# Kernel tuning notes

Measured on AMD Instinct MI355X. Metric: run time of the kernel, lower is better.

The kernel has to match this reference:

```python
import jax, jax.numpy as jnp
import numpy as np

N = 8192      # batched tree nodes
HD = 1024     # head_dim
D = 1024      # input_dim == output_dim


def _xavier(key, shape):
    fan_out, fan_in = shape
    std = (2.0 / (fan_in + fan_out)) ** 0.5
    return std * jax.random.normal(key, shape, dtype=jnp.float32)


def setup_inputs() -> dict:
    key = jax.random.key(0)
    ks = jax.random.split(key, 16)
    inp = {
        "x_l": jax.random.normal(ks[0], (N, HD), jnp.float32),
        "h_l": jax.random.normal(ks[1], (N, D), jnp.float32),
        "c_l": jax.random.normal(ks[2], (N, D), jnp.float32),
        "x_r": jax.random.normal(ks[3], (N, HD), jnp.float32),
        "h_r": jax.random.normal(ks[4], (N, D), jnp.float32),
        "c_r": jax.random.normal(ks[5], (N, D), jnp.float32),
        # Linear weights stored torch-style [out, in]; biases init to 0 per reset_parameters
        "W_i": _xavier(ks[6], (D, 4 * D)),   "b_i": jnp.zeros((D,), jnp.float32),
        "W_fl": _xavier(ks[7], (D, 4 * D)),  "b_fl": jnp.zeros((D,), jnp.float32),
        "W_fr": _xavier(ks[8], (D, 4 * D)),  "b_fr": jnp.zeros((D,), jnp.float32),
        "W_xin": _xavier(ks[9], (4 * D, HD)),
        "W_o": _xavier(ks[10], (D, 3 * D)),  "b_o": jnp.zeros((D,), jnp.float32),
        "W_z": _xavier(ks[11], (HD, 2 * HD)), "b_z": jnp.zeros((HD,), jnp.float32),
        "W_g": _xavier(ks[12], (D, 2 * D)),  "b_g": jnp.zeros((D,), jnp.float32),
        "dim": 1,
    }
    return inp


def reference(x_l, h_l, c_l, x_r, h_r, c_r,
              W_i, b_i, W_fl, b_fl, W_fr, b_fr, W_xin,
              W_o, b_o, W_z, b_z, W_g, b_g, dim):
    lin = lambda x, W, b: x @ W.T + b
    # gating to merge child head representations
    child_x = jnp.concatenate([x_l, x_r], axis=dim)
    z_t = jax.nn.sigmoid(lin(child_x, W_z, b_z))
    x_t = z_t * x_l + (1.0 - z_t) * x_r
    # input projection (no bias), split into 4 gates
    x_in_t = x_t @ W_xin.T                      # [N, 4D]
    x_i, x_f, x_o, x_g = jnp.split(x_in_t, 4, axis=dim)
    concat_input = jnp.concatenate([h_l, h_r, c_l, c_r], axis=dim)  # [N, 4D]
    i_t = jax.nn.sigmoid(lin(concat_input, W_i, b_i) + x_i)
    f_lt = jax.nn.sigmoid(lin(concat_input, W_fl, b_fl) + x_f)
    f_rt = jax.nn.sigmoid(lin(concat_input, W_fr, b_fr) + x_f)
    concat_g = jnp.concatenate([h_l, h_r], axis=dim)
    g_t = jnp.tanh(x_g + lin(concat_g, W_g, b_g))  # dropout p=0 -> identity
    c_t = f_lt * c_l + f_rt * c_r + i_t * g_t
    concat_o = jnp.concatenate([h_l, h_r, c_t], axis=dim)
    o_t = jax.nn.sigmoid(x_o + lin(concat_o, W_o, b_o))
    h_t = o_t * jnp.tanh(c_t)
    return (x_t, h_t, c_t)
```

## Files before the change

kernel.cpp:

```cpp
#include <hip/hip_runtime.h>
#include <math.h>

#define NROWS 8192

typedef __attribute__((ext_vector_type(8))) short short8;
typedef __attribute__((ext_vector_type(4))) float f32x4;
typedef __attribute__((ext_vector_type(4))) int i32x4;

__device__ __forceinline__ unsigned short f2bf(float f) {
  union { float f; unsigned int u; } v; v.f = f;
  unsigned int u = v.u;
  unsigned int r = (u + 0x7fffu + ((u >> 16) & 1u)) >> 16;
  return (unsigned short)r;
}
__device__ __forceinline__ float bf2f(unsigned short h) {
  union { unsigned int u; float f; } v; v.u = ((unsigned int)h) << 16;
  return v.f;
}
__device__ __forceinline__ float sigmoidf_(float x) { return 1.0f / (1.0f + expf(-x)); }

#define SA_INV   21.1666667f
#define SW3_INV  1016.0f
#define SWZ_INV  793.75f
#define SC_PRE3  4.64876e-5f
#define SC_ZG    5.95201e-5f

__device__ __forceinline__ unsigned char q8(float x, float inv) {
  float v = fminf(fmaxf(x * inv, -127.f), 127.f);
  return (unsigned char)(signed char)(int)rintf(v);
}

#define FENCE __builtin_amdgcn_sched_barrier(0)
#define BAR   __builtin_amdgcn_s_barrier()
#define WAIT_VM4  do { asm volatile("s_waitcnt vmcnt(4)" ::: "memory"); } while (0)
#define WAIT_VM0  do { asm volatile("s_waitcnt vmcnt(0)" ::: "memory"); } while (0)

#define LA(buf, h) (((buf) * 4 + (h)) * 8192)
#define LB(buf, h) (((buf) * 4 + 2 + (h)) * 8192)

#define GEMM_CORE                                                               \
  __shared__ unsigned short lds[65536];                                         \
  const int tid  = threadIdx.x;                                                 \
  const int wave = tid >> 6;                                                    \
  const int lane = tid & 63;                                                    \
  const int wm = wave >> 2;                                                     \
  const int wn = wave & 3;                                                      \
  const int lr = lane & 15;                                                     \
  const int kq = lane >> 4;                                                     \
  const int rsub = lane >> 3;                                                   \
  const int usw  = (lane & 7) ^ rsub;                                           \
  const int swz = (bid & 7) * (nwg >> 3) + (bid >> 3);                          \
  const int brow = (swz / nbx) * 256;                                           \
  const int bcol = (swz % nbx) * 256;                                           \
  const int nkt = K >> 6;                                                       \
  const int niter = K >> 7;                                                     \
  f32x4 acc[8][4];                                                              \
  _Pragma("unroll")                                                             \
  for (int m = 0; m < 8; ++m)                                                   \
    _Pragma("unroll")                                                           \
    for (int n = 0; n < 4; ++n)                                                 \
      acc[m][n] = (f32x4){0.f, 0.f, 0.f, 0.f};                                  \
  auto STAGE = [&](const unsigned short* src, int ld, int rowbase, int base_us, \
                   int kt) {                                                    \
    const int k0 = (kt < nkt) ? (kt << 6) : 0;                                  \
    _Pragma("unroll")                                                           \
    for (int j = 0; j < 2; ++j) {                                               \
      const int chunk = wave * 2 + j;                                           \
      const unsigned short* g =                                                 \
          src + (size_t)(rowbase + chunk * 8 + rsub) * ld + k0 + usw * 8;       \
      __builtin_amdgcn_global_load_lds(                                         \
          (const __attribute__((address_space(1))) void*)g,                     \
          (__attribute__((address_space(3))) void*)&lds[base_us + chunk * 512], \
          16, 0, 0);                                                            \
    }                                                                           \
  };                                                                            \
  short8 aM[8], aM2[8], bN[4];                                                  \
  auto LDA_ = [&](int buf, int mh, short8* d) {                                 \
    _Pragma("unroll")                                                           \
    for (int m = 0; m < 4; ++m)                                                 \
      _Pragma("unroll")                                                         \
      for (int kk = 0; kk < 2; ++kk) {                                          \
        const int r = mh * 64 + m * 16 + lr;                                    \
        const int u = (kk * 4 + kq) ^ (lr & 7);                                 \
        d[m * 2 + kk] = *(const short8*)&lds[LA(buf, wm) + r * 64 + u * 8];     \
      }                                                                         \
  };                                                                            \
  auto LDB_ = [&](int buf, int nh, short8* d) {                                 \
    _Pragma("unroll")                                                           \
    for (int n = 0; n < 2; ++n)                                                 \
      _Pragma("unroll")                                                         \
      for (int kk = 0; kk < 2; ++kk) {                                          \
        const int r = (wn & 1) * 64 + nh * 32 + n * 16 + lr;                    \
        const int u = (kk * 4 + kq) ^ (lr & 7);                                 \
        d[n * 2 + kk] = *(const short8*)&lds[LB(buf, wn >> 1) + r * 64 + u * 8];\
      }                                                                         \
  };                                                                            \
  auto MM_ = [&](int mh, int nh, short8* a, short8* b) {                        \
    _Pragma("unroll")                                                           \
    for (int m = 0; m < 4; ++m)                                                 \
      _Pragma("unroll")                                                         \
      for (int n = 0; n < 2; ++n)                                               \
        _Pragma("unroll")                                                       \
        for (int kk = 0; kk < 2; ++kk)                                          \
          acc[mh * 4 + m][nh * 2 + n] =                                         \
              __builtin_amdgcn_mfma_f32_16x16x32_bf16(                          \
                  a[m * 2 + kk], b[n * 2 + kk], acc[mh * 4 + m][nh * 2 + n],    \
                  0, 0, 0);                                                     \
  };                                                                            \
  STAGE(A, lda, brow,       LA(0, 0), 0);                                       \
  STAGE(A, lda, brow + 128, LA(0, 1), 0);                                       \
  STAGE(B, ldb, bcol,       LB(0, 0), 0);                                       \
  STAGE(B, ldb, bcol + 128, LB(0, 1), 0);                                       \
  STAGE(A, lda, brow,       LA(1, 0), 1);                                       \
  STAGE(A, lda, brow + 128, LA(1, 1), 1);                                       \
  WAIT_VM4; FENCE; BAR;                                                         \
  for (int i = 0; i < niter; ++i) {                                             \
    const int t1 = 2 * i + 1, t2 = 2 * i + 2, t3 = 2 * i + 3;                   \
    LDB_(0, 0, bN); LDA_(0, 0, aM); LDA_(0, 1, aM2);                            \
    STAGE(B, ldb, bcol,       LB(1, 0), t1);                                    \
    STAGE(B, ldb, bcol + 128, LB(1, 1), t1);                                    \
    FENCE; BAR; FENCE;                                                          \
    __builtin_amdgcn_s_setprio(1);                                              \
    MM_(0, 0, aM, bN); MM_(1, 0, aM2, bN);                                      \
    __builtin_amdgcn_s_setprio(0);                                              \
    FENCE; BAR;                                                                 \
    LDB_(0, 1, bN);                                                             \
    STAGE(A, lda, brow,       LA(0, 0), t2);                                    \
    STAGE(A, lda, brow + 128, LA(0, 1), t2);                                    \
    FENCE; BAR; FENCE;                                                          \
    __builtin_amdgcn_s_setprio(1);                                              \
    MM_(0, 1, aM, bN); MM_(1, 1, aM2, bN);                                      \
    __builtin_amdgcn_s_setprio(0);                                              \
    WAIT_VM4; FENCE; BAR;                                                       \
    LDB_(1, 0, bN); LDA_(1, 0, aM); LDA_(1, 1, aM2);                            \
    STAGE(B, ldb, bcol,       LB(0, 0), t2);                                    \
    STAGE(B, ldb, bcol + 128, LB(0, 1), t2);                                    \
    FENCE; BAR; FENCE;                                                          \
    __builtin_amdgcn_s_setprio(1);                                              \
    MM_(0, 0, aM, bN); MM_(1, 0, aM2, bN);                                      \
    __builtin_amdgcn_s_setprio(0);                                              \
    FENCE; BAR;                                                                 \
    LDB_(1, 1, bN);                                                             \
    STAGE(A, lda, brow,       LA(1, 0), t3);                                    \
    STAGE(A, lda, brow + 128, LA(1, 1), t3);                                    \
    FENCE; BAR; FENCE;                                                          \
    __builtin_amdgcn_s_setprio(1);                                              \
    MM_(0, 1, aM, bN); MM_(1, 1, aM2, bN);                                      \
    __builtin_amdgcn_s_setprio(0);                                              \
    WAIT_VM4; FENCE; BAR;                                                       \
  }                                                                             \
  WAIT_VM0;                                                                     \
  const int crow0 = brow + wm * 128 + kq * 4;                                   \
  const int ccol0 = bcol + wn * 64 + lr;

#define GEMM_STORE                                                              \
  _Pragma("unroll")                                                             \
  for (int mi = 0; mi < 8; ++mi)                                                \
    _Pragma("unroll")                                                           \
    for (int ni = 0; ni < 4; ++ni)                                              \
      _Pragma("unroll")                                                         \
      for (int j = 0; j < 4; ++j)                                               \
        C[(size_t)(crow0 + mi * 16 + j) * ldc + ccol0 + ni * 16] =              \
            f2bf(acc[mi][ni][j]);

__global__ __launch_bounds__(512) void gemm256(
    const unsigned short* __restrict__ A,
    const unsigned short* __restrict__ B,
    unsigned short* __restrict__ C,
    int K, int lda, int ldb, int ldc, int nbx)
{
  const int nwg = (int)gridDim.x;
  const int bid = (int)blockIdx.x;
  GEMM_CORE
  GEMM_STORE
}

__global__ __launch_bounds__(512) void gemm256_dual(
    const unsigned short* __restrict__ A0, const unsigned short* __restrict__ B0,
    unsigned short* __restrict__ C0, int K0, int lda0, int ldb0, int ldc0, int nbx0, int n0,
    const unsigned short* __restrict__ A1, const unsigned short* __restrict__ B1,
    unsigned short* __restrict__ C1, int K1, int lda1, int ldb1, int ldc1, int nbx1)
{
  const bool sec = ((int)blockIdx.x >= n0);
  const unsigned short* A = sec ? A1 : A0;
  const unsigned short* B = sec ? B1 : B0;
  unsigned short* C = sec ? C1 : C0;
  const int K   = sec ? K1   : K0;
  const int lda = sec ? lda1 : lda0;
  const int ldb = sec ? ldb1 : ldb0;
  const int ldc = sec ? ldc1 : ldc0;
  const int nbx = sec ? nbx1 : nbx0;
  const int nwg = sec ? ((int)gridDim.x - n0) : n0;
  const int bid = sec ? ((int)blockIdx.x - n0) : (int)blockIdx.x;
  GEMM_CORE
  GEMM_STORE
}

#define LA8(buf, h) (((buf) * 4 + (h)) * 16384)
#define LB8(buf, h) (((buf) * 4 + 2 + (h)) * 16384)

#define GEMM_CORE8                                                              \
  __shared__ unsigned char lds8[131072];                                        \
  const int tid  = threadIdx.x;                                                 \
  const int wave = tid >> 6;                                                    \
  const int lane = tid & 63;                                                    \
  const int wm = wave >> 2;                                                     \
  const int wn = wave & 3;                                                      \
  const int lr = lane & 15;                                                     \
  const int kq = lane >> 4;                                                     \
  const int rsub = lane >> 3;                                                   \
  const int usw  = (lane & 7) ^ rsub;                                           \
  const int swz = (bid & 7) * (nwg >> 3) + (bid >> 3);                          \
  const int brow = (swz / nbx) * 256;                                           \
  const int bcol = (swz % nbx) * 256;                                           \
  const int nkt = K >> 7;                                                       \
  const int niter = K >> 8;                                                     \
  i32x4 acc[8][4];                                                              \
  _Pragma("unroll")                                                             \
  for (int m = 0; m < 8; ++m)                                                   \
    _Pragma("unroll")                                                           \
    for (int n = 0; n < 4; ++n)                                                 \
      acc[m][n] = (i32x4){0, 0, 0, 0};                                          \
  auto STAGE = [&](const unsigned char* src, int ld, int rowbase, int base_b,   \
                   int kt) {                                                    \
    const int k0 = (kt < nkt) ? (kt << 7) : 0;                                  \
    _Pragma("unroll")                                                           \
    for (int j = 0; j < 2; ++j) {                                               \
      const int chunk = wave * 2 + j;                                           \
      const unsigned char* g =                                                  \
          src + (size_t)(rowbase + chunk * 8 + rsub) * ld + k0 + usw * 16;      \
      __builtin_amdgcn_global_load_lds(                                         \
          (const __attribute__((address_space(1))) void*)g,                     \
          (__attribute__((address_space(3))) void*)&lds8[base_b + chunk * 1024],\
          16, 0, 0);                                                            \
    }                                                                           \
  };                                                                            \
  i32x4 aM[8], aM2[8], bN[4];                                                   \
  auto LDA_ = [&](int buf, int mh, i32x4* d) {                                  \
    _Pragma("unroll")                                                           \
    for (int m = 0; m < 4; ++m)                                                 \
      _Pragma("unroll")                                                         \
      for (int kk = 0; kk < 2; ++kk) {                                          \
        const int r = mh * 64 + m * 16 + lr;                                    \
        const int u = (kk * 4 + kq) ^ (lr & 7);                                 \
        d[m * 2 + kk] = *(const i32x4*)&lds8[LA8(buf, wm) + r * 128 + u * 16];  \
      }                                                                         \
  };                                                                            \
  auto LDB_ = [&](int buf, int nh, i32x4* d) {                                  \
    _Pragma("unroll")                                                           \
    for (int n = 0; n < 2; ++n)                                                 \
      _Pragma("unroll")                                                         \
      for (int kk = 0; kk < 2; ++kk) {                                          \
        const int r = (wn & 1) * 64 + nh * 32 + n * 16 + lr;                    \
        const int u = (kk * 4 + kq) ^ (lr & 7);                                 \
        d[n * 2 + kk] =                                                         \
            *(const i32x4*)&lds8[LB8(buf, wn >> 1) + r * 128 + u * 16];         \
      }                                                                         \
  };                                                                            \
  auto MM_ = [&](int mh, int nh, i32x4* a, i32x4* b) {                          \
    _Pragma("unroll")                                                           \
    for (int m = 0; m < 4; ++m)                                                 \
      _Pragma("unroll")                                                         \
      for (int n = 0; n < 2; ++n)                                               \
        _Pragma("unroll")                                                       \
        for (int kk = 0; kk < 2; ++kk)                                          \
          acc[mh * 4 + m][nh * 2 + n] =                                         \
              __builtin_amdgcn_mfma_i32_16x16x64_i8(                            \
                  a[m * 2 + kk], b[n * 2 + kk], acc[mh * 4 + m][nh * 2 + n],    \
                  0, 0, 0);                                                     \
  };                                                                            \
  STAGE(A, lda, brow,       LA8(0, 0), 0);                                      \
  STAGE(A, lda, brow + 128, LA8(0, 1), 0);                                      \
  STAGE(B, ldb, bcol,       LB8(0, 0), 0);                                      \
  STAGE(B, ldb, bcol + 128, LB8(0, 1), 0);                                      \
  STAGE(A, lda, brow,       LA8(1, 0), 1);                                      \
  STAGE(A, lda, brow + 128, LA8(1, 1), 1);                                      \
  WAIT_VM4; FENCE; BAR;                                                         \
  for (int i = 0; i < niter; ++i) {                                             \
    const int t1 = 2 * i + 1, t2 = 2 * i + 2, t3 = 2 * i + 3;                   \
    LDB_(0, 0, bN); LDA_(0, 0, aM); LDA_(0, 1, aM2);                            \
    STAGE(B, ldb, bcol,       LB8(1, 0), t1);                                   \
    STAGE(B, ldb, bcol + 128, LB8(1, 1), t1);                                   \
    FENCE; BAR; FENCE;                                                          \
    __builtin_amdgcn_s_setprio(1);                                              \
    MM_(0, 0, aM, bN); MM_(1, 0, aM2, bN);                                      \
    __builtin_amdgcn_s_setprio(0);                                              \
    FENCE; BAR;                                                                 \
    LDB_(0, 1, bN);                                                             \
    STAGE(A, lda, brow,       LA8(0, 0), t2);                                   \
    STAGE(A, lda, brow + 128, LA8(0, 1), t2);                                   \
    FENCE; BAR; FENCE;                                                          \
    __builtin_amdgcn_s_setprio(1);                                              \
    MM_(0, 1, aM, bN); MM_(1, 1, aM2, bN);                                      \
    __builtin_amdgcn_s_setprio(0);                                              \
    WAIT_VM4; FENCE; BAR;                                                       \
    LDB_(1, 0, bN); LDA_(1, 0, aM); LDA_(1, 1, aM2);                            \
    STAGE(B, ldb, bcol,       LB8(0, 0), t2);                                   \
    STAGE(B, ldb, bcol + 128, LB8(0, 1), t2);                                   \
    FENCE; BAR; FENCE;                                                          \
    __builtin_amdgcn_s_setprio(1);                                              \
    MM_(0, 0, aM, bN); MM_(1, 0, aM2, bN);                                      \
    __builtin_amdgcn_s_setprio(0);                                              \
    FENCE; BAR;                                                                 \
    LDB_(1, 1, bN);                                                             \
    STAGE(A, lda, brow,       LA8(1, 0), t3);                                   \
    STAGE(A, lda, brow + 128, LA8(1, 1), t3);                                   \
    FENCE; BAR; FENCE;                                                          \
    __builtin_amdgcn_s_setprio(1);                                              \
    MM_(0, 1, aM, bN); MM_(1, 1, aM2, bN);                                      \
    __builtin_amdgcn_s_setprio(0);                                              \
    WAIT_VM4; FENCE; BAR;                                                       \
  }                                                                             \
  WAIT_VM0;                                                                     \
  const int crow0 = brow + wm * 128 + kq * 4;                                   \
  const int ccol0 = bcol + wn * 64 + lr;

__global__ __launch_bounds__(512) void gemm_ACg8(
    const unsigned char* __restrict__ A3i, const unsigned char* __restrict__ W3q,
    unsigned short* __restrict__ pre3,
    const unsigned char* __restrict__ Wgq, unsigned short* __restrict__ preg,
    const unsigned char* __restrict__ A1q, const unsigned char* __restrict__ WbZq,
    unsigned short* __restrict__ zpre)
{
  const int b = (int)blockIdx.x;
  const unsigned char* A;
  const unsigned char* B;
  unsigned short* Cb;
  int K, lda, ldb, ldc, nbx, nwg, bid;
  float cscale;
  if (b < 384) {
    A = A3i; B = W3q; Cb = pre3; K = 4096; lda = 4096; ldb = 4096; ldc = 3072;
    nbx = 12; nwg = 384; bid = b; cscale = SC_PRE3;
  } else if (b < 512) {
    A = A3i; B = Wgq; Cb = preg; K = 2048; lda = 4096; ldb = 2048; ldc = 1024;
    nbx = 4; nwg = 128; bid = b - 384; cscale = SC_ZG;
  } else {
    A = A1q; B = WbZq; Cb = zpre; K = 2048; lda = 2048; ldb = 2048; ldc = 1024;
    nbx = 4; nwg = 128; bid = b - 512; cscale = SC_ZG;
  }
  GEMM_CORE8
#pragma unroll
  for (int mi = 0; mi < 8; ++mi)
#pragma unroll
    for (int ni = 0; ni < 4; ++ni)
#pragma unroll
      for (int j = 0; j < 4; ++j)
        Cb[(size_t)(crow0 + mi * 16 + j) * ldc + ccol0 + ni * 16] =
            f2bf((float)acc[mi][ni][j] * cscale);
}

#define NB_WZ 2048
#define NB_W3 12288
#define NB_WG 2048
#define NB_A1 16384
#define NB_A3 32768

__global__ void prep_kernel(unsigned char* __restrict__ WbZq, const float* __restrict__ W_z,
                            unsigned char* __restrict__ W3q,
                            const float* __restrict__ Wi, const float* __restrict__ Wfl,
                            const float* __restrict__ Wfr,
                            unsigned char* __restrict__ Wgq, const float* __restrict__ Wg,
                            unsigned char* __restrict__ A1q,
                            const float* __restrict__ x_l, const float* __restrict__ x_r,
                            unsigned short* __restrict__ A3,
                            unsigned char* __restrict__ A3i,
                            const float* __restrict__ h_l, const float* __restrict__ h_r,
                            const float* __restrict__ c_l, const float* __restrict__ c_r)
{
  int b = (int)blockIdx.x;
  if (b < NB_WZ) {
    size_t idx = ((size_t)b * 256 + threadIdx.x) * 4;
    float4 v = *(const float4*)&W_z[idx];
    uchar4 q;
    q.x = q8(v.x, SWZ_INV); q.y = q8(v.y, SWZ_INV);
    q.z = q8(v.z, SWZ_INV); q.w = q8(v.w, SWZ_INV);
    *(uchar4*)&WbZq[idx] = q;
  } else if (b < NB_WZ + NB_W3) {
    size_t idx = ((size_t)(b - NB_WZ) * 256 + threadIdx.x) * 4;
    int m = (int)(idx >> 12);
    int k = (int)(idx & 4095);
    const float* W = (m < 1024) ? Wi : (m < 2048) ? Wfl : Wfr;
    float4 v = *(const float4*)&W[(size_t)(m & 1023) * 4096 + k];
    uchar4 q;
    q.x = q8(v.x, SW3_INV); q.y = q8(v.y, SW3_INV);
    q.z = q8(v.z, SW3_INV); q.w = q8(v.w, SW3_INV);
    *(uchar4*)&W3q[idx] = q;
  } else if (b < NB_WZ + NB_W3 + NB_WG) {
    size_t idx = ((size_t)(b - NB_WZ - NB_W3) * 256 + threadIdx.x) * 4;
    float4 v = *(const float4*)&Wg[idx];
    uchar4 q;
    q.x = q8(v.x, SWZ_INV); q.y = q8(v.y, SWZ_INV);
    q.z = q8(v.z, SWZ_INV); q.w = q8(v.w, SWZ_INV);
    *(uchar4*)&Wgq[idx] = q;
  } else if (b < NB_WZ + NB_W3 + NB_WG + NB_A1) {
    size_t idx = ((size_t)(b - NB_WZ - NB_W3 - NB_WG) * 256 + threadIdx.x) * 4;
    size_t n = idx >> 11;
    int rem = (int)(idx & 2047);
    const float* s = (rem < 1024) ? x_l : x_r;
    float4 v = *(const float4*)&s[(n << 10) + (rem & 1023)];
    uchar4 q;
    q.x = q8(v.x, SA_INV); q.y = q8(v.y, SA_INV);
    q.z = q8(v.z, SA_INV); q.w = q8(v.w, SA_INV);
    *(uchar4*)&A1q[idx] = q;
  } else {
    size_t idx = ((size_t)(b - NB_WZ - NB_W3 - NB_WG - NB_A1) * 256 + threadIdx.x) * 4;
    size_t n = idx >> 12;
    int rem = (int)(idx & 4095);
    int i = rem >> 10;
    const float* s = (i == 0) ? h_l : (i == 1) ? h_r : (i == 2) ? c_l : c_r;
    float4 v = *(const float4*)&s[(n << 10) + (rem & 1023)];
    ushort4 o;
    o.x = f2bf(v.x); o.y = f2bf(v.y); o.z = f2bf(v.z); o.w = f2bf(v.w);
    *(ushort4*)&A3[idx] = o;
    uchar4 q;
    q.x = q8(v.x, SA_INV); q.y = q8(v.y, SA_INV);
    q.z = q8(v.z, SA_INV); q.w = q8(v.w, SA_INV);
    *(uchar4*)&A3i[idx] = q;
  }
}

#define NB_EW1 8192
__global__ void ew1wx_kernel(const unsigned short* __restrict__ zp,
                             const float* __restrict__ bz,
                             const float* __restrict__ xl, const float* __restrict__ xr,
                             float* __restrict__ out_x, unsigned short* __restrict__ A2,
                             unsigned short* __restrict__ Wx, const float* __restrict__ W_xin)
{
  int b = (int)blockIdx.x;
  if (b < NB_EW1) {
    size_t idx = ((size_t)b * 256 + threadIdx.x) * 4;
    int j = (int)(idx & 1023);
    ushort4 z4 = *(const ushort4*)&zp[idx];
    float4 bz4 = *(const float4*)&bz[j];
    float4 xl4 = *(const float4*)&xl[idx];
    float4 xr4 = *(const float4*)&xr[idx];
    float4 xo;
    ushort4 ao;
    float z, xt;
    z = sigmoidf_(bf2f(z4.x) + bz4.x); xt = z * xl4.x + (1.f - z) * xr4.x; xo.x = xt; ao.x = f2bf(xt);
    z = sigmoidf_(bf2f(z4.y) + bz4.y); xt = z * xl4.y + (1.f - z) * xr4.y; xo.y = xt; ao.y = f2bf(xt);
    z = sigmoidf_(bf2f(z4.z) + bz4.z); xt = z * xl4.z + (1.f - z) * xr4.z; xo.z = xt; ao.z = f2bf(xt);
    z = sigmoidf_(bf2f(z4.w) + bz4.w); xt = z * xl4.w + (1.f - z) * xr4.w; xo.w = xt; ao.w = f2bf(xt);
    *(float4*)&out_x[idx] = xo;
    *(ushort4*)&A2[idx] = ao;
  } else {
    size_t idx = ((size_t)(b - NB_EW1) * 256 + threadIdx.x) * 4;
    float4 v = *(const float4*)&W_xin[idx];
    ushort4 o;
    o.x = f2bf(v.x); o.y = f2bf(v.y); o.z = f2bf(v.z); o.w = f2bf(v.w);
    *(ushort4*)&Wx[idx] = o;
  }
}

#define NB_EW2 8192
__global__ void ew2wo_kernel(const unsigned short* __restrict__ pre3,
                             const unsigned short* __restrict__ preg,
                             const unsigned short* __restrict__ xin,
                             const float* __restrict__ b_i, const float* __restrict__ b_fl,
                             const float* __restrict__ b_fr, const float* __restrict__ b_g,
                             float* __restrict__ out_c, unsigned short* __restrict__ A3,
                             unsigned short* __restrict__ Wo, const float* __restrict__ W_o)
{
  int b = (int)blockIdx.x;
  if (b < NB_EW2) {
    size_t idx = ((size_t)b * 256 + threadIdx.x) * 4;
    int j = (int)(idx & 1023);
    size_t n = idx >> 10;
    size_t r3 = n * 3072;
    size_t r4 = n << 12;
    ushort4 pi = *(const ushort4*)&pre3[r3 + j];
    ushort4 pf1 = *(const ushort4*)&pre3[r3 + 1024 + j];
    ushort4 pf2 = *(const ushort4*)&pre3[r3 + 2048 + j];
    ushort4 pg = *(const ushort4*)&preg[idx];
    ushort4 xi = *(const ushort4*)&xin[r4 + j];
    ushort4 xf = *(const ushort4*)&xin[r4 + 1024 + j];
    ushort4 xg = *(const ushort4*)&xin[r4 + 3072 + j];
    ushort4 cl4 = *(const ushort4*)&A3[r4 + 2048 + j];
    ushort4 cr4 = *(const ushort4*)&A3[r4 + 3072 + j];
    float4 bi4 = *(const float4*)&b_i[j];
    float4 bfl4 = *(const float4*)&b_fl[j];
    float4 bfr4 = *(const float4*)&b_fr[j];
    float4 bg4 = *(const float4*)&b_g[j];
    float4 co;
    ushort4 ao;
#define EW2_ONE(pi_, pf1_, pf2_, pg_, xi_, xf_, xg_, bi_, bfl_, bfr_, bg_, cl_, cr_, oc_, oa_) \
    { float xiv = bf2f(xi_), xfv = bf2f(xf_), xgv = bf2f(xg_);                                 \
      float it = sigmoidf_(bf2f(pi_) + bi_ + xiv);                                             \
      float fl = sigmoidf_(bf2f(pf1_) + bfl_ + xfv);                                           \
      float fr = sigmoidf_(bf2f(pf2_) + bfr_ + xfv);                                           \
      float g  = tanhf(bf2f(pg_) + bg_ + xgv);                                                 \
      float c_ = fl * bf2f(cl_) + fr * bf2f(cr_) + it * g;                                     \
      oc_ = c_; oa_ = f2bf(c_); }
    EW2_ONE(pi.x, pf1.x, pf2.x, pg.x, xi.x, xf.x, xg.x, bi4.x, bfl4.x, bfr4.x, bg4.x, cl4.x, cr4.x, co.x, ao.x)
    EW2_ONE(pi.y, pf1.y, pf2.y, pg.y, xi.y, xf.y, xg.y, bi4.y, bfl4.y, bfr4.y, bg4.y, cl4.y, cr4.y, co.y, ao.y)
    EW2_ONE(pi.z, pf1.z, pf2.z, pg.z, xi.z, xf.z, xg.z, bi4.z, bfl4.z, bfr4.z, bg4.z, cl4.z, cr4.z, co.z, ao.z)
    EW2_ONE(pi.w, pf1.w, pf2.w, pg.w, xi.w, xf.w, xg.w, bi4.w, bfl4.w, bfr4.w, bg4.w, cl4.w, cr4.w, co.w, ao.w)
#undef EW2_ONE
    *(float4*)&out_c[idx] = co;
    *(ushort4*)&A3[r4 + 2048 + j] = ao;
  } else {
    size_t idx = ((size_t)(b - NB_EW2) * 256 + threadIdx.x) * 4;
    float4 v = *(const float4*)&W_o[idx];
    ushort4 o;
    o.x = f2bf(v.x); o.y = f2bf(v.y); o.z = f2bf(v.z); o.w = f2bf(v.w);
    *(ushort4*)&Wo[idx] = o;
  }
}

__global__ void ew3_kernel(const unsigned short* __restrict__ op0,
                           const unsigned short* __restrict__ op1,
                           const float* __restrict__ b_o,
                           const unsigned short* __restrict__ xin,
                           const unsigned short* __restrict__ A3,
                           float* __restrict__ out_h)
{
  size_t idx = ((size_t)blockIdx.x * 256 + threadIdx.x) * 4;
  int j = (int)(idx & 1023);
  size_t n = idx >> 10;
  ushort4 opa = *(const ushort4*)&op0[idx];
  ushort4 opb = *(const ushort4*)&op1[idx];
  ushort4 xo = *(const ushort4*)&xin[(n << 12) + 2048 + j];
  ushort4 ct4 = *(const ushort4*)&A3[(n << 12) + 2048 + j];
  float4 bo4 = *(const float4*)&b_o[j];
  float4 ho;
  ho.x = sigmoidf_(bf2f(opa.x) + bf2f(opb.x) + bo4.x + bf2f(xo.x)) * tanhf(bf2f(ct4.x));
  ho.y = sigmoidf_(bf2f(opa.y) + bf2f(opb.y) + bo4.y + bf2f(xo.y)) * tanhf(bf2f(ct4.y));
  ho.z = sigmoidf_(bf2f(opa.z) + bf2f(opb.z) + bo4.z + bf2f(xo.z)) * tanhf(bf2f(ct4.z));
  ho.w = sigmoidf_(bf2f(opa.w) + bf2f(opb.w) + bo4.w + bf2f(xo.w)) * tanhf(bf2f(ct4.w));
  *(float4*)&out_h[idx] = ho;
}

extern "C" void kernel_launch(void* const* d_in, const int* in_sizes, int n_in,
                              void* d_out, int out_size, void* d_ws, size_t ws_size,
                              hipStream_t stream)
{
  const float* x_l  = (const float*)d_in[0];
  const float* h_l  = (const float*)d_in[1];
  const float* c_l  = (const float*)d_in[2];
  const float* x_r  = (const float*)d_in[3];
  const float* h_r  = (const float*)d_in[4];
  const float* c_r  = (const float*)d_in[5];
  const float* W_i  = (const float*)d_in[6];
  const float* b_i  = (const float*)d_in[7];
  const float* W_fl = (const float*)d_in[8];
  const float* b_fl = (const float*)d_in[9];
  const float* W_fr = (const float*)d_in[10];
  const float* b_fr = (const float*)d_in[11];
  const float* W_xin= (const float*)d_in[12];
  const float* W_o  = (const float*)d_in[13];
  const float* b_o  = (const float*)d_in[14];
  const float* W_z  = (const float*)d_in[15];
  const float* b_z  = (const float*)d_in[16];
  const float* W_g  = (const float*)d_in[17];
  const float* b_g  = (const float*)d_in[18];

  float* out_x = (float*)d_out;
  float* out_h = out_x + (size_t)NROWS * 1024;
  float* out_c = out_x + 2 * (size_t)NROWS * 1024;

  char* ws = (char*)d_ws;
  unsigned char*  A1q  = (unsigned char*)ws;
  unsigned char*  WbZq = (unsigned char*)(ws + 16777216);
  unsigned char*  W3q  = (unsigned char*)(ws + 18874368);
  unsigned char*  Wgq  = (unsigned char*)(ws + 31457280);
  unsigned char*  A3i  = (unsigned char*)(ws + 33554432);
  unsigned short* A3   = (unsigned short*)(ws + 67108864);
  unsigned short* zpre = (unsigned short*)(ws + 134217728);
  unsigned short* A2   = (unsigned short*)(ws + 134217728);
  unsigned short* Wo   = (unsigned short*)(ws + 134217728);
  unsigned short* pre3 = (unsigned short*)(ws + 150994944);
  unsigned short* opre0= (unsigned short*)(ws + 150994944);
  unsigned short* opre1= (unsigned short*)(ws + 167772160);
  unsigned short* preg = (unsigned short*)(ws + 201326592);
  unsigned short* Wx   = (unsigned short*)(ws + 218103808);
  unsigned short* xin  = (unsigned short*)ws;

  const dim3 blk(256);
  const dim3 gblk(512);

  prep_kernel<<<dim3(NB_WZ + NB_W3 + NB_WG + NB_A1 + NB_A3), blk, 0, stream>>>(
      WbZq, W_z, W3q, W_i, W_fl, W_fr, Wgq, W_g, A1q, x_l, x_r,
      A3, A3i, h_l, h_r, c_l, c_r);

  gemm_ACg8<<<dim3(640), gblk, 0, stream>>>(A3i, W3q, pre3, Wgq, preg, A1q, WbZq, zpre);

  ew1wx_kernel<<<dim3(NB_EW1 + 4096), blk, 0, stream>>>(
      zpre, b_z, x_l, x_r, out_x, A2, Wx, W_xin);

  gemm256<<<dim3(16 * (NROWS / 256)), gblk, 0, stream>>>(A2, Wx, xin, 1024, 1024, 1024, 4096, 16);

  ew2wo_kernel<<<dim3(NB_EW2 + 3072), blk, 0, stream>>>(
      pre3, preg, xin, b_i, b_fl, b_fr, b_g, out_c, A3, Wo, W_o);

  gemm256_dual<<<dim3(256), gblk, 0, stream>>>(
      A3, Wo, opre0, 1536, 4096, 3072, 1024, 4, 128,
      A3 + 1536, Wo + 1536, opre1, 1536, 4096, 3072, 1024, 4);

  ew3_kernel<<<dim3(NB_EW1), blk, 0, stream>>>(opre0, opre1, b_o, xin, A3, out_h);
}
```

Baseline: 397.7 us.

## Run output-gate GEMM in int8/fp8 quantized path and shrink bf16 staging

Replaces the bf16 dual GEMM for the output gate with an 8-bit quantized GEMM (gemm_D8) that reuses the already-quantized A3i buffer and a quantized W_o. c_t is written into A3i in quantized form, and the bf16 copy is kept only for c_l, c_r and c_t in a smaller Ac buffer. The prep kernel no longer writes the full bf16 A3. This cuts memory traffic and raises matrix throughput, at the cost of lower precision for the o-gate preactivation. The workspace layout is reshuffled to fit the new buffers.

```diff
diff --git a/kernel.cpp b/kernel.cpp
--- a/kernel.cpp
+++ b/kernel.cpp
@@ -153,16 +153,6 @@
   const int crow0 = brow + wm * 128 + kq * 4;                                   \
   const int ccol0 = bcol + wn * 64 + lr;
 
-#define GEMM_STORE                                                              \
-  _Pragma("unroll")                                                             \
-  for (int mi = 0; mi < 8; ++mi)                                                \
-    _Pragma("unroll")                                                           \
-    for (int ni = 0; ni < 4; ++ni)                                              \
-      _Pragma("unroll")                                                         \
-      for (int j = 0; j < 4; ++j)                                               \
-        C[(size_t)(crow0 + mi * 16 + j) * ldc + ccol0 + ni * 16] =              \
-            f2bf(acc[mi][ni][j]);
-
 __global__ __launch_bounds__(512) void gemm256(
     const unsigned short* __restrict__ A,
     const unsigned short* __restrict__ B,
@@ -172,28 +162,13 @@
   const int nwg = (int)gridDim.x;
   const int bid = (int)blockIdx.x;
   GEMM_CORE
-  GEMM_STORE
-}
-
-__global__ __launch_bounds__(512) void gemm256_dual(
-    const unsigned short* __restrict__ A0, const unsigned short* __restrict__ B0,
-    unsigned short* __restrict__ C0, int K0, int lda0, int ldb0, int ldc0, int nbx0, int n0,
-    const unsigned short* __restrict__ A1, const unsigned short* __restrict__ B1,
-    unsigned short* __restrict__ C1, int K1, int lda1, int ldb1, int ldc1, int nbx1)
-{
-  const bool sec = ((int)blockIdx.x >= n0);
-  const unsigned short* A = sec ? A1 : A0;
-  const unsigned short* B = sec ? B1 : B0;
-  unsigned short* C = sec ? C1 : C0;
-  const int K   = sec ? K1   : K0;
-  const int lda = sec ? lda1 : lda0;
-  const int ldb = sec ? ldb1 : ldb0;
-  const int ldc = sec ? ldc1 : ldc0;
-  const int nbx = sec ? nbx1 : nbx0;
-  const int nwg = sec ? ((int)gridDim.x - n0) : n0;
-  const int bid = sec ? ((int)blockIdx.x - n0) : (int)blockIdx.x;
-  GEMM_CORE
-  GEMM_STORE
+#pragma unroll
+  for (int mi = 0; mi < 8; ++mi)
+#pragma unroll
+    for (int ni = 0; ni < 4; ++ni)
+#pragma unroll
+      for (int j = 0; j < 4; ++j)
+        C[(size_t)(crow0 + mi * 16 + j) * ldc + ccol0 + ni * 16] = f2bf(acc[mi][ni][j]);
 }
 
 #define LA8(buf, h) (((buf) * 4 + (h)) * 16384)
@@ -349,6 +324,28 @@
             f2bf((float)acc[mi][ni][j] * cscale);
 }
 
+__global__ __launch_bounds__(512) void gemm_D8(
+    const unsigned char* __restrict__ A3i, const unsigned char* __restrict__ Woq,
+    unsigned short* __restrict__ opre0, unsigned short* __restrict__ opre1)
+{
+  const int b = (int)blockIdx.x;
+  const bool sec = (b >= 128);
+  const unsigned char* A = A3i + (sec ? 1536 : 0);
+  const unsigned char* B = Woq + (sec ? 1536 : 0);
+  unsigned short* Cb = sec ? opre1 : opre0;
+  const int K = 1536, lda = 4096, ldb = 3072, ldc = 1024, nbx = 4, nwg = 128;
+  const int bid = sec ? b - 128 : b;
+  GEMM_CORE8
+#pragma unroll
+  for (int mi = 0; mi < 8; ++mi)
+#pragma unroll
+    for (int ni = 0; ni < 4; ++ni)
+#pragma unroll
+      for (int j = 0; j < 4; ++j)
+        Cb[(size_t)(crow0 + mi * 16 + j) * ldc + ccol0 + ni * 16] =
+            f2bf((float)acc[mi][ni][j] * SC_ZG);
+}
+
 #define NB_WZ 2048
 #define NB_W3 12288
 #define NB_WG 2048
@@ -362,7 +359,7 @@
                             unsigned char* __restrict__ Wgq, const float* __restrict__ Wg,
                             unsigned char* __restrict__ A1q,
                             const float* __restrict__ x_l, const float* __restrict__ x_r,
-                            unsigned short* __restrict__ A3,
+                            unsigned short* __restrict__ Ac,
                             unsigned char* __restrict__ A3i,
                             const float* __restrict__ h_l, const float* __restrict__ h_r,
                             const float* __restrict__ c_l, const float* __restrict__ c_r)
@@ -407,15 +404,18 @@
     size_t n = idx >> 12;
     int rem = (int)(idx & 4095);
     int i = rem >> 10;
+    int j = rem & 1023;
     const float* s = (i == 0) ? h_l : (i == 1) ? h_r : (i == 2) ? c_l : c_r;
-    float4 v = *(const float4*)&s[(n << 10) + (rem & 1023)];
-    ushort4 o;
-    o.x = f2bf(v.x); o.y = f2bf(v.y); o.z = f2bf(v.z); o.w = f2bf(v.w);
-    *(ushort4*)&A3[idx] = o;
+    float4 v = *(const float4*)&s[(n << 10) + j];
     uchar4 q;
     q.x = q8(v.x, SA_INV); q.y = q8(v.y, SA_INV);
     q.z = q8(v.z, SA_INV); q.w = q8(v.w, SA_INV);
     *(uchar4*)&A3i[idx] = q;
+    if (i >= 2) {
+      ushort4 o;
+      o.x = f2bf(v.x); o.y = f2bf(v.y); o.z = f2bf(v.z); o.w = f2bf(v.w);
+      *(ushort4*)&Ac[n * 2048 + (i - 2) * 1024 + j] = o;
+    }
   }
 }
 
@@ -458,8 +458,9 @@
                              const unsigned short* __restrict__ xin,
                              const float* __restrict__ b_i, const float* __restrict__ b_fl,
                              const float* __restrict__ b_fr, const float* __restrict__ b_g,
-                             float* __restrict__ out_c, unsigned short* __restrict__ A3,
-                             unsigned short* __restrict__ Wo, const float* __restrict__ W_o)
+                             float* __restrict__ out_c, unsigned short* __restrict__ Ac,
+                             unsigned char* __restrict__ A3i,
+                             unsigned char* __restrict__ Woq, const float* __restrict__ W_o)
 {
   int b = (int)blockIdx.x;
   if (b < NB_EW2) {
@@ -468,6 +469,7 @@
     size_t n = idx >> 10;
     size_t r3 = n * 3072;
     size_t r4 = n << 12;
+    size_t r2 = n << 11;
     ushort4 pi = *(const ushort4*)&pre3[r3 + j];
     ushort4 pf1 = *(const ushort4*)&pre3[r3 + 1024 + j];
     ushort4 pf2 = *(const ushort4*)&pre3[r3 + 2048 + j];
@@ -475,35 +477,38 @@
     ushort4 xi = *(const ushort4*)&xin[r4 + j];
     ushort4 xf = *(const ushort4*)&xin[r4 + 1024 + j];
     ushort4 xg = *(const ushort4*)&xin[r4 + 3072 + j];
-    ushort4 cl4 = *(const ushort4*)&A3[r4 + 2048 + j];
-    ushort4 cr4 = *(const ushort4*)&A3[r4 + 3072 + j];
+    ushort4 cl4 = *(const ushort4*)&Ac[r2 + j];
+    ushort4 cr4 = *(const ushort4*)&Ac[r2 + 1024 + j];
     float4 bi4 = *(const float4*)&b_i[j];
     float4 bfl4 = *(const float4*)&b_fl[j];
     float4 bfr4 = *(const float4*)&b_fr[j];
     float4 bg4 = *(const float4*)&b_g[j];
     float4 co;
     ushort4 ao;
-#define EW2_ONE(pi_, pf1_, pf2_, pg_, xi_, xf_, xg_, bi_, bfl_, bfr_, bg_, cl_, cr_, oc_, oa_) \
-    { float xiv = bf2f(xi_), xfv = bf2f(xf_), xgv = bf2f(xg_);                                 \
-      float it = sigmoidf_(bf2f(pi_) + bi_ + xiv);                                             \
-      float fl = sigmoidf_(bf2f(pf1_) + bfl_ + xfv);                                           \
-      float fr = sigmoidf_(bf2f(pf2_) + bfr_ + xfv);                                           \
-      float g  = tanhf(bf2f(pg_) + bg_ + xgv);                                                 \
-      float c_ = fl * bf2f(cl_) + fr * bf2f(cr_) + it * g;                                     \
-      oc_ = c_; oa_ = f2bf(c_); }
-    EW2_ONE(pi.x, pf1.x, pf2.x, pg.x, xi.x, xf.x, xg.x, bi4.x, bfl4.x, bfr4.x, bg4.x, cl4.x, cr4.x, co.x, ao.x)
-    EW2_ONE(pi.y, pf1.y, pf2.y, pg.y, xi.y, xf.y, xg.y, bi4.y, bfl4.y, bfr4.y, bg4.y, cl4.y, cr4.y, co.y, ao.y)
-    EW2_ONE(pi.z, pf1.z, pf2.z, pg.z, xi.z, xf.z, xg.z, bi4.z, bfl4.z, bfr4.z, bg4.z, cl4.z, cr4.z, co.z, ao.z)
-    EW2_ONE(pi.w, pf1.w, pf2.w, pg.w, xi.w, xf.w, xg.w, bi4.w, bfl4.w, bfr4.w, bg4.w, cl4.w, cr4.w, co.w, ao.w)
+    uchar4 aq;
+#define EW2_ONE(pi_, pf1_, pf2_, pg_, xi_, xf_, xg_, bi_, bfl_, bfr_, bg_, cl_, cr_, oc_, oa_, oq_) \
+    { float xiv = bf2f(xi_), xfv = bf2f(xf_), xgv = bf2f(xg_);                                      \
+      float it = sigmoidf_(bf2f(pi_) + bi_ + xiv);                                                  \
+      float fl = sigmoidf_(bf2f(pf1_) + bfl_ + xfv);                                                \
+      float fr = sigmoidf_(bf2f(pf2_) + bfr_ + xfv);                                                \
+      float g  = tanhf(bf2f(pg_) + bg_ + xgv);                                                      \
+      float c_ = fl * bf2f(cl_) + fr * bf2f(cr_) + it * g;                                          \
+      oc_ = c_; oa_ = f2bf(c_); oq_ = q8(c_, SA_INV); }
+    EW2_ONE(pi.x, pf1.x, pf2.x, pg.x, xi.x, xf.x, xg.x, bi4.x, bfl4.x, bfr4.x, bg4.x, cl4.x, cr4.x, co.x, ao.x, aq.x)
+    EW2_ONE(pi.y, pf1.y, pf2.y, pg.y, xi.y, xf.y, xg.y, bi4.y, bfl4.y, bfr4.y, bg4.y, cl4.y, cr4.y, co.y, ao.y, aq.y)
+    EW2_ONE(pi.z, pf1.z, pf2.z, pg.z, xi.z, xf.z, xg.z, bi4.z, bfl4.z, bfr4.z, bg4.z, cl4.z, cr4.z, co.z, ao.z, aq.z)
+    EW2_ONE(pi.w, pf1.w, pf2.w, pg.w, xi.w, xf.w, xg.w, bi4.w, bfl4.w, bfr4.w, bg4.w, cl4.w, cr4.w, co.w, ao.w, aq.w)
 #undef EW2_ONE
     *(float4*)&out_c[idx] = co;
-    *(ushort4*)&A3[r4 + 2048 + j] = ao;
+    *(ushort4*)&Ac[r2 + j] = ao;
+    *(uchar4*)&A3i[r4 + 2048 + j] = aq;
   } else {
     size_t idx = ((size_t)(b - NB_EW2) * 256 + threadIdx.x) * 4;
     float4 v = *(const float4*)&W_o[idx];
-    ushort4 o;
-    o.x = f2bf(v.x); o.y = f2bf(v.y); o.z = f2bf(v.z); o.w = f2bf(v.w);
-    *(ushort4*)&Wo[idx] = o;
+    uchar4 q;
+    q.x = q8(v.x, SWZ_INV); q.y = q8(v.y, SWZ_INV);
+    q.z = q8(v.z, SWZ_INV); q.w = q8(v.w, SWZ_INV);
+    *(uchar4*)&Woq[idx] = q;
   }
 }
 
@@ -511,7 +516,7 @@
                            const unsigned short* __restrict__ op1,
                            const float* __restrict__ b_o,
                            const unsigned short* __restrict__ xin,
-                           const unsigned short* __restrict__ A3,
+                           const unsigned short* __restrict__ Ac,
                            float* __restrict__ out_h)
 {
   size_t idx = ((size_t)blockIdx.x * 256 + threadIdx.x) * 4;
@@ -520,7 +525,7 @@
   ushort4 opa = *(const ushort4*)&op0[idx];
   ushort4 opb = *(const ushort4*)&op1[idx];
   ushort4 xo = *(const ushort4*)&xin[(n << 12) + 2048 + j];
-  ushort4 ct4 = *(const ushort4*)&A3[(n << 12) + 2048 + j];
+  ushort4 ct4 = *(const ushort4*)&Ac[(n << 11) + j];
   float4 bo4 = *(const float4*)&b_o[j];
   float4 ho;
   ho.x = sigmoidf_(bf2f(opa.x) + bf2f(opb.x) + bo4.x + bf2f(xo.x)) * tanhf(bf2f(ct4.x));
@@ -560,27 +565,27 @@
 
   char* ws = (char*)d_ws;
   unsigned char*  A1q  = (unsigned char*)ws;
-  unsigned char*  WbZq = (unsigned char*)(ws + 16777216);
-  unsigned char*  W3q  = (unsigned char*)(ws + 18874368);
-  unsigned char*  Wgq  = (unsigned char*)(ws + 31457280);
-  unsigned char*  A3i  = (unsigned char*)(ws + 33554432);
-  unsigned short* A3   = (unsigned short*)(ws + 67108864);
+  unsigned short* xin  = (unsigned short*)ws;
+  unsigned char*  A3i  = (unsigned char*)(ws + 67108864);
+  unsigned short* Ac   = (unsigned short*)(ws + 100663296);
   unsigned short* zpre = (unsigned short*)(ws + 134217728);
   unsigned short* A2   = (unsigned short*)(ws + 134217728);
-  unsigned short* Wo   = (unsigned short*)(ws + 134217728);
-  unsigned short* pre3 = (unsigned short*)(ws + 150994944);
+  unsigned char*  Woq  = (unsigned char*)(ws + 134217728);
+  unsigned char*  WbZq = (unsigned char*)(ws + 150994944);
+  unsigned char*  W3q  = (unsigned char*)(ws + 153092096);
+  unsigned char*  Wgq  = (unsigned char*)(ws + 165675008);
+  unsigned short* Wx   = (unsigned short*)(ws + 150994944);
   unsigned short* opre0= (unsigned short*)(ws + 150994944);
+  unsigned short* preg = (unsigned short*)(ws + 167772160);
   unsigned short* opre1= (unsigned short*)(ws + 167772160);
-  unsigned short* preg = (unsigned short*)(ws + 201326592);
-  unsigned short* Wx   = (unsigned short*)(ws + 218103808);
-  unsigned short* xin  = (unsigned short*)ws;
+  unsigned short* pre3 = (unsigned short*)(ws + 184549376);
 
   const dim3 blk(256);
   const dim3 gblk(512);
 
   prep_kernel<<<dim3(NB_WZ + NB_W3 + NB_WG + NB_A1 + NB_A3), blk, 0, stream>>>(
       WbZq, W_z, W3q, W_i, W_fl, W_fr, Wgq, W_g, A1q, x_l, x_r,
-      A3, A3i, h_l, h_r, c_l, c_r);
+      Ac, A3i, h_l, h_r, c_l, c_r);
 
   gemm_ACg8<<<dim3(640), gblk, 0, stream>>>(A3i, W3q, pre3, Wgq, preg, A1q, WbZq, zpre);
 
@@ -590,11 +595,9 @@
   gemm256<<<dim3(16 * (NROWS / 256)), gblk, 0, stream>>>(A2, Wx, xin, 1024, 1024, 1024, 4096, 16);
 
   ew2wo_kernel<<<dim3(NB_EW2 + 3072), blk, 0, stream>>>(
-      pre3, preg, xin, b_i, b_fl, b_fr, b_g, out_c, A3, Wo, W_o);
-
-  gemm256_dual<<<dim3(256), gblk, 0, stream>>>(
-      A3, Wo, opre0, 1536, 4096, 3072, 1024, 4, 128,
-      A3 + 1536, Wo + 1536, opre1, 1536, 4096, 3072, 1024, 4);
-
-  ew3_kernel<<<dim3(NB_EW1), blk, 0, stream>>>(opre0, opre1, b_o, xin, A3, out_h);
-}
+      pre3, preg, xin, b_i, b_fl, b_fr, b_g, out_c, Ac, A3i, Woq, W_o);
+
+  gemm_D8<<<dim3(256), gblk, 0, stream>>>(A3i, Woq, opre0, opre1);
+
+  ew3_kernel<<<dim3(NB_EW1), blk, 0, stream>>>(opre0, opre1, b_o, xin, Ac, out_h);
+}
```

Measured after the change: 377.9 us. 1.05x faster.
